# Kernel optimization log

Hardware: AMD Instinct MI355X
Metric: run time of the kernel (lower is better)

Reference implementation:

```python
import jax, jax.numpy as jnp
import numpy as np

CHANNELS = 512
GROUPS = 32
EPS = 1e-6


def setup_inputs() -> dict:
    key = jax.random.key(0)
    ks = jax.random.split(key, 10)
    C = CHANNELS
    s = 1.0 / np.sqrt(C)
    return {
        "hidden_states": jax.random.normal(ks[0], (4, 64, 64, C), dtype=jnp.float32),
        "gn_scale": jnp.ones((C,), dtype=jnp.float32),
        "gn_bias": jnp.zeros((C,), dtype=jnp.float32),
        "wq": jax.random.normal(ks[1], (C, C), dtype=jnp.float32) * s,
        "bq": jnp.zeros((C,), dtype=jnp.float32),
        "wk": jax.random.normal(ks[2], (C, C), dtype=jnp.float32) * s,
        "bk": jnp.zeros((C,), dtype=jnp.float32),
        "wv": jax.random.normal(ks[3], (C, C), dtype=jnp.float32) * s,
        "bv": jnp.zeros((C,), dtype=jnp.float32),
        "wo": jax.random.normal(ks[4], (C, C), dtype=jnp.float32) * s,
        "bo": jnp.zeros((C,), dtype=jnp.float32),
    }


def reference(hidden_states, gn_scale, gn_bias, wq, bq, wk, bk, wv, bv, wo, bo):
    B, H, W, C = hidden_states.shape
    residual = hidden_states
    L = H * W
    x = hidden_states.reshape(B, L, C)

    # GroupNorm: stats over (spatial, channels-within-group), per batch per group
    xg = x.reshape(B, L, GROUPS, C // GROUPS)
    mean = jnp.mean(xg, axis=(1, 3), keepdims=True)
    var = jnp.var(xg, axis=(1, 3), keepdims=True)
    xn = ((xg - mean) * jax.lax.rsqrt(var + EPS)).reshape(B, L, C)
    xn = xn * gn_scale + gn_bias

    # QKV projections (heads=1, head_dim=C)
    q = xn @ wq + bq
    k = xn @ wk + bk
    v = xn @ wv + bv

    scale = 1.0 / jnp.sqrt(jnp.asarray(C, dtype=q.dtype))
    scores = jnp.einsum('bld,bsd->bls', q, k) * scale  # [B, L, L]
    attn = jax.nn.softmax(scores, axis=-1)
    out = jnp.einsum('bls,bsd->bld', attn, v)

    out = out @ wo + bo
    return out.reshape(B, H, W, C) + residual
```

## Files before the change

kernel.cpp:

```cpp
#include <hip/hip_runtime.h>
#include <hip/hip_bf16.h>
#include <stdint.h>

#define BATCH 4
#define SEQ   4096
#define CH    512
#define NGRP  32
#define GEPS  1e-6f

typedef short  short8  __attribute__((ext_vector_type(8)));
typedef float  floatx4 __attribute__((ext_vector_type(4)));
typedef long   longx2  __attribute__((ext_vector_type(2)));

static __device__ __forceinline__ short bf16b(float f) {
    __hip_bfloat16 h = __float2bfloat16(f);
    return __builtin_bit_cast(short, h);
}
static __device__ __forceinline__ float bf2f(short s) {
    unsigned u = ((unsigned)(unsigned short)s) << 16;
    return __builtin_bit_cast(float, u);
}
static __device__ __forceinline__ char fp8b(float f) {
    int pk = __builtin_amdgcn_cvt_pk_fp8_f32(f, f, 0, false);
    return (char)(pk & 0xff);
}

static __device__ __forceinline__ void dma16(const void* g, void* l) {
    __builtin_amdgcn_global_load_lds(
        (const __attribute__((address_space(1))) unsigned int*)g,
        (__attribute__((address_space(3))) unsigned int*)l, 16, 0, 0);
}

static __device__ __forceinline__ float rowmax16(float x) {
    int xi = __builtin_bit_cast(int, x);
    x = fmaxf(x, __builtin_bit_cast(float, __builtin_amdgcn_update_dpp(xi, xi, 0x128, 0xf, 0xf, true)));
    xi = __builtin_bit_cast(int, x);
    x = fmaxf(x, __builtin_bit_cast(float, __builtin_amdgcn_update_dpp(xi, xi, 0x124, 0xf, 0xf, true)));
    xi = __builtin_bit_cast(int, x);
    x = fmaxf(x, __builtin_bit_cast(float, __builtin_amdgcn_update_dpp(xi, xi, 0x122, 0xf, 0xf, true)));
    xi = __builtin_bit_cast(int, x);
    x = fmaxf(x, __builtin_bit_cast(float, __builtin_amdgcn_update_dpp(xi, xi, 0x121, 0xf, 0xf, true)));
    return x;
}

__global__ __launch_bounds__(256) void gn_partial_kernel(const float* __restrict__ x,
                                                         float* __restrict__ statsraw) {
    int blk = blockIdx.x;
    int t = threadIdx.x;
    size_t row0 = (size_t)blk * 64;
    int qd = t & 127;
    int rh = t >> 7;
    const float* base = x + row0 * 512 + qd * 4;
    float s1 = 0.f, s2 = 0.f;
    #pragma unroll 4
    for (int i = 0; i < 32; ++i) {
        int r = rh + i * 2;
        float4 v = *reinterpret_cast<const float4*>(base + (size_t)r * 512);
        s1 += v.x + v.y + v.z + v.w;
        s2 += v.x * v.x + v.y * v.y + v.z * v.z + v.w * v.w;
    }
    __shared__ float a1[256], a2[256];
    a1[t] = s1; a2[t] = s2;
    __syncthreads();
    if (t < 32) {
        float u1 = 0.f, u2 = 0.f;
        #pragma unroll
        for (int e = 0; e < 4; ++e) {
            u1 += a1[t * 4 + e] + a1[128 + t * 4 + e];
            u2 += a2[t * 4 + e] + a2[128 + t * 4 + e];
        }
        int b = (int)(row0 >> 12);
        atomicAdd(&statsraw[(b * 32 + t) * 2],     u1);
        atomicAdd(&statsraw[(b * 32 + t) * 2 + 1], u2);
    }
}

__global__ __launch_bounds__(256) void gn_apply_kernel(const float* __restrict__ x,
                                                       const float* __restrict__ statsraw,
                                                       const float* __restrict__ gsc,
                                                       const float* __restrict__ gbs,
                                                       short* __restrict__ xn) {
    int i4 = blockIdx.x * 256 + threadIdx.x;
    int base = i4 * 4;
    int b = base >> 21;
    int c = base & 511;
    int sidx = (b * 32 + (c >> 4)) * 2;
    float s1 = statsraw[sidx], s2 = statsraw[sidx + 1];
    float mean = s1 * (1.f / 65536.f);
    float var  = s2 * (1.f / 65536.f) - mean * mean;
    float rstd = rsqrtf(var + GEPS);
    float4 xv = reinterpret_cast<const float4*>(x)[i4];
    float4 sv = *reinterpret_cast<const float4*>(gsc + c);
    float4 bv = *reinterpret_cast<const float4*>(gbs + c);
    union { short s[4]; uint2 u; } p;
    p.s[0] = bf16b((xv.x - mean) * rstd * sv.x + bv.x);
    p.s[1] = bf16b((xv.y - mean) * rstd * sv.y + bv.y);
    p.s[2] = bf16b((xv.z - mean) * rstd * sv.z + bv.z);
    p.s[3] = bf16b((xv.w - mean) * rstd * sv.w + bv.w);
    reinterpret_cast<uint2*>(xn)[i4] = p.u;
}

__global__ __launch_bounds__(256) void wtrans_kernel(const float* __restrict__ w0,
                                                     const float* __restrict__ w1,
                                                     const float* __restrict__ w2,
                                                     const float* __restrict__ w3,
                                                     short* __restrict__ wT) {
    const float* w = (blockIdx.z == 0) ? w0 : (blockIdx.z == 1) ? w1
                   : (blockIdx.z == 2) ? w2 : w3;
    short* out = wT + (size_t)blockIdx.z * CH * CH;
    int n0 = blockIdx.x * 32, k0 = blockIdx.y * 32;
    int tx = threadIdx.x, ty = threadIdx.y;
    __shared__ float s[32][33];
    #pragma unroll
    for (int i = 0; i < 4; ++i) {
        int kk = ty + i * 8;
        s[kk][tx] = w[(size_t)(k0 + kk) * CH + n0 + tx];
    }
    __syncthreads();
    #pragma unroll
    for (int i = 0; i < 4; ++i) {
        int nn = ty + i * 8;
        out[(size_t)(n0 + nn) * CH + k0 + tx] = bf16b(s[tx][nn]);
    }
}

__global__ __launch_bounds__(256) void gemm_qkv_kernel(const short* __restrict__ A,
                                                       const short* __restrict__ wT,
                                                       const float* __restrict__ bq,
                                                       const float* __restrict__ bk,
                                                       const float* __restrict__ bv,
                                                       char* __restrict__ q8,
                                                       char* __restrict__ k8,
                                                       char* __restrict__ vT8) {
    __shared__ short As[128 * 64];
    __shared__ short Bs[128 * 64];
    __shared__ char  vls[128 * 144];
    int m0 = blockIdx.x * 128;
    int nblk = blockIdx.y;
    int which = nblk >> 2;
    int n0 = (nblk & 3) * 128;
    const short* BT = wT + (size_t)which * 512 * 512;
    const float* bias = (which == 0) ? bq : (which == 1) ? bk : bv;
    int t = threadIdx.x;
    int w = t >> 6, lane = t & 63;
    int wr = w >> 1, wc = w & 1;
    int l15 = lane & 15, l4 = lane >> 4;
    floatx4 acc[4][4];
    #pragma unroll
    for (int i = 0; i < 4; ++i)
        #pragma unroll
        for (int j = 0; j < 4; ++j) acc[i][j] = (floatx4){0.f, 0.f, 0.f, 0.f};

    for (int k0 = 0; k0 < 512; k0 += 64) {
        __syncthreads();
        #pragma unroll
        for (int i = 0; i < 4; ++i) {
            int c = i * 256 + t;
            int row = c >> 3, j = (c & 7) ^ (row & 7);
            dma16(&A[(size_t)(m0 + row) * 512 + k0 + j * 8], &As[(c & ~63) * 8]);
            dma16(&BT[(size_t)(n0 + row) * 512 + k0 + j * 8], &Bs[(c & ~63) * 8]);
        }
        __syncthreads();
        #pragma unroll
        for (int kk = 0; kk < 64; kk += 32) {
            short8 af[4], bf[4];
            #pragma unroll
            for (int i = 0; i < 4; ++i) {
                int row = wr * 64 + i * 16 + l15;
                int j = (kk >> 3) + l4;
                af[i] = *reinterpret_cast<const short8*>(&As[(row * 8 + (j ^ (l15 & 7))) * 8]);
            }
            #pragma unroll
            for (int j2 = 0; j2 < 4; ++j2) {
                int row = wc * 64 + j2 * 16 + l15;
                int j = (kk >> 3) + l4;
                bf[j2] = *reinterpret_cast<const short8*>(&Bs[(row * 8 + (j ^ (l15 & 7))) * 8]);
            }
            #pragma unroll
            for (int i = 0; i < 4; ++i)
                #pragma unroll
                for (int j2 = 0; j2 < 4; ++j2)
                    acc[i][j2] = __builtin_amdgcn_mfma_f32_16x16x32_bf16(af[i], bf[j2], acc[i][j2], 0, 0, 0);
        }
    }
    if (which == 0) {
        #pragma unroll
        for (int i = 0; i < 4; ++i)
            #pragma unroll
            for (int j = 0; j < 4; ++j)
                #pragma unroll
                for (int r = 0; r < 4; ++r) {
                    int row = m0 + wr * 64 + i * 16 + l4 * 4 + r;
                    int col = n0 + wc * 64 + j * 16 + l15;
                    q8[(size_t)row * 512 + col] = fp8b(acc[i][j][r] + bias[col]);
                }
    } else if (which == 1) {
        #pragma unroll
        for (int i = 0; i < 4; ++i)
            #pragma unroll
            for (int j = 0; j < 4; ++j)
                #pragma unroll
                for (int r = 0; r < 4; ++r) {
                    int row = m0 + wr * 64 + i * 16 + l4 * 4 + r;
                    int col = n0 + wc * 64 + j * 16 + l15;
                    int bb = row >> 12, s = row & 4095;
                    size_t idx = (size_t)bb * 2097152 + (size_t)(s >> 5) * 16384
                               + (s & 15) * 1024 + ((s >> 4) & 1) * 8
                               + (col >> 3) * 16 + (col & 7);
                    k8[idx] = fp8b(acc[i][j][r] + bias[col]);
                }
    } else {
        __syncthreads();
        #pragma unroll
        for (int i = 0; i < 4; ++i)
            #pragma unroll
            for (int j = 0; j < 4; ++j)
                #pragma unroll
                for (int r = 0; r < 4; ++r) {
                    int rl = wr * 64 + i * 16 + l4 * 4 + r;
                    int rp = (rl & ~31) | (((rl & 15) << 1) | ((rl >> 4) & 1));
                    int cl = wc * 64 + j * 16 + l15;
                    vls[cl * 144 + rp] = fp8b(acc[i][j][r] + bias[n0 + cl]);
                }
        __syncthreads();
        int b = m0 >> 12, l0 = m0 & 4095;
        #pragma unroll
        for (int p = 0; p < 4; ++p) {
            int slot = p * 256 + t;
            int c = slot >> 3, off = (slot & 7) * 16;
            uint4 v;
            __builtin_memcpy(&v, &vls[c * 144 + off], 16);
            int dcol = n0 + c;
            int g = dcol >> 5, rr = dcol & 15, h = (dcol >> 4) & 1;
            int s = l0 + off;
            int sb = s >> 5, mb = (s & 31) >> 3;
            char* dst = vT8 + (size_t)b * 2097152 + (size_t)sb * 16384
                      + (size_t)((((g * 16 + rr) * 4 + mb) * 16) + h * 8);
            unsigned long long lo = ((unsigned long long)v.y << 32) | v.x;
            unsigned long long hi = ((unsigned long long)v.w << 32) | v.z;
            *reinterpret_cast<unsigned long long*>(dst)      = lo;
            *reinterpret_cast<unsigned long long*>(dst + 16) = hi;
        }
    }
}

__global__ __launch_bounds__(256) void gemm_bt_kernel(const short* __restrict__ Opart,
                                                      const float* __restrict__ ml,
                                                      const short* __restrict__ BT,
                                                      const float* __restrict__ bias,
                                                      float* __restrict__ outf,
                                                      const float* __restrict__ resid) {
    __shared__ short As[128 * 64];
    __shared__ short Bs[128 * 64];
    int m0 = blockIdx.x * 128, n0 = blockIdx.y * 128;
    int t = threadIdx.x;
    int w = t >> 6, lane = t & 63;
    int wr = w >> 1, wc = w & 1;
    int l15 = lane & 15, l4 = lane >> 4;
    const size_t PART = (size_t)BATCH * SEQ;
    floatx4 acc[4][4];
    #pragma unroll
    for (int i = 0; i < 4; ++i)
        #pragma unroll
        for (int j = 0; j < 4; ++j) acc[i][j] = (floatx4){0.f, 0.f, 0.f, 0.f};

    for (int k0 = 0; k0 < 512; k0 += 64) {
        __syncthreads();
        #pragma unroll
        for (int i = 0; i < 4; ++i) {
            int c = i * 256 + t;
            int rl = c >> 3, j = (c & 7) ^ (rl & 7);
            size_t rowg = (size_t)(m0 + rl);
            const short* s0 = Opart + rowg * 512 + k0 + j * 8;
            const short* s1 = s0 + PART * 512;
            uint4 a0 = *reinterpret_cast<const uint4*>(s0);
            uint4 a1 = *reinterpret_cast<const uint4*>(s1);
            float mA = ml[rowg * 2],          lA = ml[rowg * 2 + 1];
            float mB = ml[(PART + rowg) * 2], lB = ml[(PART + rowg) * 2 + 1];
            float mm = fmaxf(mA, mB);
            float e0 = __expf(mA - mm), e1 = __expf(mB - mm);
            float inv = 1.f / (e0 * lA + e1 * lB);
            e0 *= inv; e1 *= inv;
            union { uint4 u; short s[8]; } ua, ub, uo;
            ua.u = a0; ub.u = a1;
            #pragma unroll
            for (int e = 0; e < 8; ++e)
                uo.s[e] = bf16b(bf2f(ua.s[e]) * e0 + bf2f(ub.s[e]) * e1);
            *reinterpret_cast<uint4*>(&As[c * 8]) = uo.u;
            dma16(&BT[(size_t)(n0 + rl) * 512 + k0 + j * 8], &Bs[(c & ~63) * 8]);
        }
        __syncthreads();
        #pragma unroll
        for (int kk = 0; kk < 64; kk += 32) {
            short8 af[4], bf[4];
            #pragma unroll
            for (int i = 0; i < 4; ++i) {
                int row = wr * 64 + i * 16 + l15;
                int j = (kk >> 3) + l4;
                af[i] = *reinterpret_cast<const short8*>(&As[(row * 8 + (j ^ (l15 & 7))) * 8]);
            }
            #pragma unroll
            for (int j2 = 0; j2 < 4; ++j2) {
                int row = wc * 64 + j2 * 16 + l15;
                int j = (kk >> 3) + l4;
                bf[j2] = *reinterpret_cast<const short8*>(&Bs[(row * 8 + (j ^ (l15 & 7))) * 8]);
            }
            #pragma unroll
            for (int i = 0; i < 4; ++i)
                #pragma unroll
                for (int j2 = 0; j2 < 4; ++j2)
                    acc[i][j2] = __builtin_amdgcn_mfma_f32_16x16x32_bf16(af[i], bf[j2], acc[i][j2], 0, 0, 0);
        }
    }
    #pragma unroll
    for (int i = 0; i < 4; ++i)
        #pragma unroll
        for (int j = 0; j < 4; ++j)
            #pragma unroll
            for (int r = 0; r < 4; ++r) {
                int row = m0 + wr * 64 + i * 16 + l4 * 4 + r;
                int col = n0 + wc * 64 + j * 16 + l15;
                float vv = acc[i][j][r] + bias[col];
                outf[(size_t)row * 512 + col] = vv + resid[(size_t)row * 512 + col];
            }
}

__global__ __launch_bounds__(256, 2) void flash_kernel(const char* __restrict__ q8,
                                                       const char* __restrict__ k8,
                                                       const char* __restrict__ v8,
                                                       short* __restrict__ Opart,
                                                       float* __restrict__ ml) {
    __shared__ __align__(16) char smem[68096];
    int bx = blockIdx.x;
    int pb = bx & 7;
    int part = pb >> 2, b = pb & 3;
    int q0 = (bx >> 3) * 64;
    int t = threadIdx.x, w = t >> 6, lane = t & 63;
    int l15 = lane & 15, l4 = lane >> 4;
    const float scale = 0.044194173824159216f;

    long qf[16];
    {
        const char* qrow = q8 + ((size_t)b * SEQ + q0 + w * 16 + l15) * 512;
        #pragma unroll
        for (int ks = 0; ks < 16; ++ks)
            qf[ks] = *reinterpret_cast<const long*>(qrow + ks * 32 + l4 * 8);
    }

    floatx4 acc[32];
    #pragma unroll
    for (int i = 0; i < 32; ++i) acc[i] = (floatx4){0.f, 0.f, 0.f, 0.f};
    floatx4 lacc = (floatx4){0.f, 0.f, 0.f, 0.f};
    float mused[4] = {-1e30f, -1e30f, -1e30f, -1e30f};

    const long ones = 0x3838383838383838L;

    const char* kbase = k8 + (size_t)b * SEQ * 512;
    const char* vbase = v8 + (size_t)b * 512 * SEQ;

    const int ksw = l15 & 7;
    const int vsw = (l15 >> 1) & 3;
    const int sb0 = part * 64;

    auto stage = [&](int sb, int buf) {
        char* Kd = smem + buf * 16384;
        char* Vd = smem + 32768 + buf * 16384;
        const char* kt = kbase + (size_t)sb * 16384;
        const char* vt = vbase + (size_t)sb * 16384;
        #pragma unroll
        for (int i = 0; i < 4; ++i) {
            int c = i * 256 + t;
            int src = (c & ~63) | ((c & 63) ^ ((c >> 6) & 7));
            dma16(kt + (size_t)src * 16, Kd + (size_t)(c & ~63) * 16);
        }
        #pragma unroll
        for (int i = 0; i < 4; ++i) {
            int c = i * 256 + t;
            int src = (c & ~3) | ((c & 3) ^ ((c >> 3) & 3));
            dma16(vt + (size_t)src * 16, Vd + (size_t)(c & ~63) * 16);
        }
    };

    stage(sb0, 0);
    __syncthreads();

    for (int it = 0; it < 64; ++it) {
        int cur = it & 1;
        if (it + 1 < 64) stage(sb0 + it + 1, 1 - cur);

        const char* Kb = smem + cur * 16384;
        const char* Vb = smem + 32768 + cur * 16384;

        floatx4 sa0 = (floatx4){0.f, 0.f, 0.f, 0.f};
        floatx4 sa1 = (floatx4){0.f, 0.f, 0.f, 0.f};
        #pragma unroll
        for (int ks = 0; ks < 16; ++ks) {
            longx2 kk = *reinterpret_cast<const longx2*>(
                Kb + ((l15 * 64 + ((ks * 4 + l4) ^ ksw)) << 4));
            sa0 = __builtin_amdgcn_mfma_f32_16x16x32_fp8_fp8(qf[ks], kk[0], sa0, 0, 0, 0);
            sa1 = __builtin_amdgcn_mfma_f32_16x16x32_fp8_fp8(qf[ks], kk[1], sa1, 0, 0, 0);
        }

        float v0[4], v1[4], nm4[4];
        bool need = false;
        #pragma unroll
        for (int r = 0; r < 4; ++r) {
            v0[r] = sa0[r] * scale; v1[r] = sa1[r] * scale;
            nm4[r] = rowmax16(fmaxf(v0[r], v1[r]));
            need |= (nm4[r] > mused[r] + 5.0f);
        }
        if (__ballot(need)) {
            #pragma unroll
            for (int r = 0; r < 4; ++r) {
                float nm = fmaxf(mused[r], nm4[r]);
                float al = __expf(mused[r] - nm);
                lacc[r] *= al;
                #pragma unroll
                for (int i = 0; i < 32; ++i) acc[i][r] *= al;
                mused[r] = nm;
            }
        }
        float p0[4], p1[4];
        #pragma unroll
        for (int r = 0; r < 4; ++r) {
            p0[r] = __expf(v0[r] - mused[r]);
            p1[r] = __expf(v1[r] - mused[r]);
        }

        char* Ps = smem + 65536 + w * 640;
        #pragma unroll
        for (int r = 0; r < 4; ++r) {
            int pk = __builtin_amdgcn_cvt_pk_fp8_f32(p0[r], p1[r], 0, false);
            *reinterpret_cast<short*>(Ps + (l4 * 4 + r) * 40 + l15 * 2) = (short)pk;
        }

        long pf;
        __builtin_memcpy(&pf, (const char*)__builtin_assume_aligned(Ps + l15 * 40 + l4 * 8, 8), 8);
        lacc = __builtin_amdgcn_mfma_f32_16x16x32_fp8_fp8(pf, ones, lacc, 0, 0, 0);
        #pragma unroll
        for (int g = 0; g < 16; ++g) {
            longx2 vv = *reinterpret_cast<const longx2*>(
                Vb + ((((g * 16 + l15) * 4) + (l4 ^ vsw)) << 4));
            acc[2 * g]     = __builtin_amdgcn_mfma_f32_16x16x32_fp8_fp8(pf, vv[0], acc[2 * g],     0, 0, 0);
            acc[2 * g + 1] = __builtin_amdgcn_mfma_f32_16x16x32_fp8_fp8(pf, vv[1], acc[2 * g + 1], 0, 0, 0);
        }

        __syncthreads();
    }

    short* obase = Opart + (((size_t)part * BATCH + b) * SEQ + q0 + w * 16) * 512;
    #pragma unroll
    for (int r = 0; r < 4; ++r) {
        #pragma unroll
        for (int tt = 0; tt < 32; ++tt)
            obase[(size_t)(l4 * 4 + r) * 512 + tt * 16 + l15] = bf16b(acc[tt][r]);
    }
    if (l15 == 0) {
        #pragma unroll
        for (int r = 0; r < 4; ++r) {
            size_t rowg = ((size_t)part * BATCH + b) * SEQ + q0 + w * 16 + l4 * 4 + r;
            ml[rowg * 2]     = mused[r];
            ml[rowg * 2 + 1] = lacc[r];
        }
    }
}

extern "C" void kernel_launch(void* const* d_in, const int* in_sizes, int n_in,
                              void* d_out, int out_size, void* d_ws, size_t ws_size,
                              hipStream_t stream) {
    const float* x   = (const float*)d_in[0];
    const float* gsc = (const float*)d_in[1];
    const float* gbs = (const float*)d_in[2];
    const float* wq  = (const float*)d_in[3];
    const float* bq  = (const float*)d_in[4];
    const float* wk  = (const float*)d_in[5];
    const float* bk  = (const float*)d_in[6];
    const float* wv  = (const float*)d_in[7];
    const float* bv  = (const float*)d_in[8];
    const float* wo  = (const float*)d_in[9];
    const float* bo  = (const float*)d_in[10];
    float* out = (float*)d_out;

    char* ws = (char*)d_ws;
    const size_t MB = 1ull << 20;
    short* xn    = (short*)ws;
    char*  q8    = (char*)(ws + 16 * MB);
    char*  k8    = (char*)(ws + 24 * MB);
    char*  vT8   = (char*)(ws + 32 * MB);
    short* Opart = (short*)(ws + 40 * MB);
    short* wT    = (short*)(ws + 72 * MB);
    float* stats = (float*)(ws + 74 * MB);
    float* ml    = (float*)(ws + 74 * MB + 65536);

    hipMemsetAsync(stats, 0, 256 * sizeof(float), stream);
    gn_partial_kernel<<<256, 256, 0, stream>>>(x, stats);
    gn_apply_kernel<<<8192, 256, 0, stream>>>(x, stats, gsc, gbs, xn);
    wtrans_kernel<<<dim3(16, 16, 4), dim3(32, 8), 0, stream>>>(wq, wk, wv, wo, wT);

    short* woT = wT + 786432;

    gemm_qkv_kernel<<<dim3(128, 12), 256, 0, stream>>>(xn, wT, bq, bk, bv, q8, k8, vT8);
    flash_kernel<<<512, 256, 0, stream>>>(q8, k8, vT8, Opart, ml);
    gemm_bt_kernel<<<dim3(128, 4), 256, 0, stream>>>(Opart, ml, woT, bo, out, x);
}
```

Measured before the change: 289.0 us.

## Software-pipeline flash attention: overlap QK^T of next tile with PV of current

```diff
diff --git a/kernel.cpp b/kernel.cpp
--- a/kernel.cpp
+++ b/kernel.cpp
@@ -278,7 +278,7 @@
             float mA = ml[rowg * 2],          lA = ml[rowg * 2 + 1];
             float mB = ml[(PART + rowg) * 2], lB = ml[(PART + rowg) * 2 + 1];
             float mm = fmaxf(mA, mB);
-            float e0 = __expf(mA - mm), e1 = __expf(mB - mm);
+            float e0 = exp2f(mA - mm), e1 = exp2f(mB - mm);
             float inv = 1.f / (e0 * lA + e1 * lB);
             e0 *= inv; e1 *= inv;
             union { uint4 u; short s[8]; } ua, ub, uo;
@@ -337,7 +337,8 @@
     int q0 = (bx >> 3) * 64;
     int t = threadIdx.x, w = t >> 6, lane = t & 63;
     int l15 = lane & 15, l4 = lane >> 4;
-    const float scale = 0.044194173824159216f;
+    const float c2 = 0.06375873735f;
+    const float MARGIN = 7.2134752f;
 
     long qf[16];
     {
@@ -357,22 +358,27 @@
 
     const char* kbase = k8 + (size_t)b * SEQ * 512;
     const char* vbase = v8 + (size_t)b * 512 * SEQ;
+    const int sb0 = part * 64;
 
     const int ksw = l15 & 7;
     const int vsw = (l15 >> 1) & 3;
-    const int sb0 = part * 64;
-
-    auto stage = [&](int sb, int buf) {
-        char* Kd = smem + buf * 16384;
-        char* Vd = smem + 32768 + buf * 16384;
+    const char* kAddrE = smem + ((l15 * 64 + (l4 ^ ksw)) << 4);
+    const char* kAddrO = smem + ((l15 * 64 + ((4 + l4) ^ ksw)) << 4);
+    const int vLane = (l15 * 4 + (l4 ^ vsw)) << 4;
+    char* Ps = smem + 65536 + w * 640;
+
+    auto stageK = [&](int sb) {
         const char* kt = kbase + (size_t)sb * 16384;
-        const char* vt = vbase + (size_t)sb * 16384;
         #pragma unroll
         for (int i = 0; i < 4; ++i) {
             int c = i * 256 + t;
             int src = (c & ~63) | ((c & 63) ^ ((c >> 6) & 7));
-            dma16(kt + (size_t)src * 16, Kd + (size_t)(c & ~63) * 16);
-        }
+            dma16(kt + (size_t)src * 16, smem + (size_t)(c & ~63) * 16);
+        }
+    };
+    auto stageV = [&](int sb, int vOff) {
+        const char* vt = vbase + (size_t)sb * 16384;
+        char* Vd = smem + vOff;
         #pragma unroll
         for (int i = 0; i < 4; ++i) {
             int c = i * 256 + t;
@@ -380,73 +386,99 @@
             dma16(vt + (size_t)src * 16, Vd + (size_t)(c & ~63) * 16);
         }
     };
-
-    stage(sb0, 0);
-    __syncthreads();
-
-    for (int it = 0; it < 64; ++it) {
-        int cur = it & 1;
-        if (it + 1 < 64) stage(sb0 + it + 1, 1 - cur);
-
-        const char* Kb = smem + cur * 16384;
-        const char* Vb = smem + 32768 + cur * 16384;
-
-        floatx4 sa0 = (floatx4){0.f, 0.f, 0.f, 0.f};
-        floatx4 sa1 = (floatx4){0.f, 0.f, 0.f, 0.f};
-        #pragma unroll
-        for (int ks = 0; ks < 16; ++ks) {
-            longx2 kk = *reinterpret_cast<const longx2*>(
-                Kb + ((l15 * 64 + ((ks * 4 + l4) ^ ksw)) << 4));
-            sa0 = __builtin_amdgcn_mfma_f32_16x16x32_fp8_fp8(qf[ks], kk[0], sa0, 0, 0, 0);
-            sa1 = __builtin_amdgcn_mfma_f32_16x16x32_fp8_fp8(qf[ks], kk[1], sa1, 0, 0, 0);
-        }
-
+    auto qkt = [&](floatx4& sa0, floatx4& sa1) {
+        __builtin_amdgcn_s_setprio(1);
+        #pragma unroll
+        for (int j = 0; j < 8; ++j) {
+            longx2 kE = *reinterpret_cast<const longx2*>(kAddrE + j * 128);
+            longx2 kO = *reinterpret_cast<const longx2*>(kAddrO + j * 128);
+            sa0 = __builtin_amdgcn_mfma_f32_16x16x32_fp8_fp8(qf[2 * j],     kE[0], sa0, 0, 0, 0);
+            sa1 = __builtin_amdgcn_mfma_f32_16x16x32_fp8_fp8(qf[2 * j],     kE[1], sa1, 0, 0, 0);
+            sa0 = __builtin_amdgcn_mfma_f32_16x16x32_fp8_fp8(qf[2 * j + 1], kO[0], sa0, 0, 0, 0);
+            sa1 = __builtin_amdgcn_mfma_f32_16x16x32_fp8_fp8(qf[2 * j + 1], kO[1], sa1, 0, 0, 0);
+        }
+        __builtin_amdgcn_s_setprio(0);
+    };
+    auto pv = [&](long pfv, int vRd) {
+        __builtin_amdgcn_s_setprio(1);
+        lacc = __builtin_amdgcn_mfma_f32_16x16x32_fp8_fp8(pfv, ones, lacc, 0, 0, 0);
+        const char* Vb = smem + vRd;
+        #pragma unroll
+        for (int g = 0; g < 16; ++g) {
+            longx2 vv = *reinterpret_cast<const longx2*>(Vb + vLane + g * 1024);
+            acc[2 * g]     = __builtin_amdgcn_mfma_f32_16x16x32_fp8_fp8(pfv, vv[0], acc[2 * g],     0, 0, 0);
+            acc[2 * g + 1] = __builtin_amdgcn_mfma_f32_16x16x32_fp8_fp8(pfv, vv[1], acc[2 * g + 1], 0, 0, 0);
+        }
+        __builtin_amdgcn_s_setprio(0);
+    };
+    auto softmax = [&](floatx4 sa0, floatx4 sa1) -> long {
         float v0[4], v1[4], nm4[4];
         bool need = false;
         #pragma unroll
         for (int r = 0; r < 4; ++r) {
-            v0[r] = sa0[r] * scale; v1[r] = sa1[r] * scale;
+            v0[r] = sa0[r] * c2; v1[r] = sa1[r] * c2;
             nm4[r] = rowmax16(fmaxf(v0[r], v1[r]));
-            need |= (nm4[r] > mused[r] + 5.0f);
+            need |= (nm4[r] > mused[r] + MARGIN);
+        }
+        #pragma unroll
+        for (int r = 0; r < 4; ++r) {
+            int pk = __builtin_amdgcn_cvt_pk_fp8_f32(exp2f(v0[r] - mused[r]),
+                                                     exp2f(v1[r] - mused[r]), 0, false);
+            *reinterpret_cast<short*>(Ps + (l4 * 4 + r) * 40 + l15 * 2) = (short)pk;
         }
         if (__ballot(need)) {
             #pragma unroll
             for (int r = 0; r < 4; ++r) {
                 float nm = fmaxf(mused[r], nm4[r]);
-                float al = __expf(mused[r] - nm);
+                float al = exp2f(mused[r] - nm);
                 lacc[r] *= al;
                 #pragma unroll
                 for (int i = 0; i < 32; ++i) acc[i][r] *= al;
                 mused[r] = nm;
+                int pk = __builtin_amdgcn_cvt_pk_fp8_f32(exp2f(v0[r] - nm),
+                                                         exp2f(v1[r] - nm), 0, false);
+                *reinterpret_cast<short*>(Ps + (l4 * 4 + r) * 40 + l15 * 2) = (short)pk;
             }
         }
-        float p0[4], p1[4];
-        #pragma unroll
-        for (int r = 0; r < 4; ++r) {
-            p0[r] = __expf(v0[r] - mused[r]);
-            p1[r] = __expf(v1[r] - mused[r]);
-        }
-
-        char* Ps = smem + 65536 + w * 640;
-        #pragma unroll
-        for (int r = 0; r < 4; ++r) {
-            int pk = __builtin_amdgcn_cvt_pk_fp8_f32(p0[r], p1[r], 0, false);
-            *reinterpret_cast<short*>(Ps + (l4 * 4 + r) * 40 + l15 * 2) = (short)pk;
-        }
-
-        long pf;
-        __builtin_memcpy(&pf, (const char*)__builtin_assume_aligned(Ps + l15 * 40 + l4 * 8, 8), 8);
-        lacc = __builtin_amdgcn_mfma_f32_16x16x32_fp8_fp8(pf, ones, lacc, 0, 0, 0);
-        #pragma unroll
-        for (int g = 0; g < 16; ++g) {
-            longx2 vv = *reinterpret_cast<const longx2*>(
-                Vb + ((((g * 16 + l15) * 4) + (l4 ^ vsw)) << 4));
-            acc[2 * g]     = __builtin_amdgcn_mfma_f32_16x16x32_fp8_fp8(pf, vv[0], acc[2 * g],     0, 0, 0);
-            acc[2 * g + 1] = __builtin_amdgcn_mfma_f32_16x16x32_fp8_fp8(pf, vv[1], acc[2 * g + 1], 0, 0, 0);
-        }
-
-        __syncthreads();
-    }
+        long pfv;
+        __builtin_memcpy(&pfv, (const char*)__builtin_assume_aligned(Ps + l15 * 40 + l4 * 8, 8), 8);
+        return pfv;
+    };
+
+    stageV(sb0, 16384);
+    stageK(sb0);
+    asm volatile("s_waitcnt vmcnt(0)" ::: "memory");
+    __syncthreads();
+
+    long pf;
+    {
+        stageV(sb0 + 1, 32768);
+        floatx4 sa0 = (floatx4){0.f, 0.f, 0.f, 0.f};
+        floatx4 sa1 = (floatx4){0.f, 0.f, 0.f, 0.f};
+        qkt(sa0, sa1);
+        __syncthreads();
+        stageK(sb0 + 1);
+        pf = softmax(sa0, sa1);
+        asm volatile("s_waitcnt vmcnt(0)" ::: "memory");
+        __syncthreads();
+    }
+    int vRd = 16384;
+    int vWr = 49152;
+    for (int it = 1; it < 64; ++it) {
+        if (it + 1 < 64) stageV(sb0 + it + 1, vWr);
+        floatx4 sa0 = (floatx4){0.f, 0.f, 0.f, 0.f};
+        floatx4 sa1 = (floatx4){0.f, 0.f, 0.f, 0.f};
+        qkt(sa0, sa1);
+        __syncthreads();
+        if (it + 1 < 64) stageK(sb0 + it + 1);
+        pv(pf, vRd);
+        pf = softmax(sa0, sa1);
+        asm volatile("s_waitcnt vmcnt(0)" ::: "memory");
+        __syncthreads();
+        vRd = (vRd == 49152) ? 16384 : vRd + 16384;
+        vWr = (vWr == 49152) ? 16384 : vWr + 16384;
+    }
+    pv(pf, vRd);
 
     short* obase = Opart + (((size_t)part * BATCH + b) * SEQ + q0 + w * 16) * 512;
     #pragma unroll
```

After: 294.8 us. +2.0%, slower.

## Use exp2 softmax, precompute LDS addresses, and raise MFMA wave priority

Applied to the files above, without the earlier changes.

```diff
diff --git a/kernel.cpp b/kernel.cpp
--- a/kernel.cpp
+++ b/kernel.cpp
@@ -278,7 +278,7 @@
             float mA = ml[rowg * 2],          lA = ml[rowg * 2 + 1];
             float mB = ml[(PART + rowg) * 2], lB = ml[(PART + rowg) * 2 + 1];
             float mm = fmaxf(mA, mB);
-            float e0 = __expf(mA - mm), e1 = __expf(mB - mm);
+            float e0 = exp2f(mA - mm), e1 = exp2f(mB - mm);
             float inv = 1.f / (e0 * lA + e1 * lB);
             e0 *= inv; e1 *= inv;
             union { uint4 u; short s[8]; } ua, ub, uo;
@@ -337,7 +337,8 @@
     int q0 = (bx >> 3) * 64;
     int t = threadIdx.x, w = t >> 6, lane = t & 63;
     int l15 = lane & 15, l4 = lane >> 4;
-    const float scale = 0.044194173824159216f;
+    const float c2 = 0.06375873735f;
+    const float MARGIN = 7.2134752f;
 
     long qf[16];
     {
@@ -357,28 +358,33 @@
 
     const char* kbase = k8 + (size_t)b * SEQ * 512;
     const char* vbase = v8 + (size_t)b * 512 * SEQ;
+    const int sb0 = part * 64;
 
     const int ksw = l15 & 7;
     const int vsw = (l15 >> 1) & 3;
-    const int sb0 = part * 64;
+    const char* kA_E = smem + ((l15 * 64 + (l4 ^ ksw)) << 4);
+    const char* kA_O = smem + ((l15 * 64 + ((4 + l4) ^ ksw)) << 4);
+    const char* vA   = smem + 32768 + ((l15 * 4 + (l4 ^ vsw)) << 4);
+    char* Ps = smem + 65536 + w * 640;
+
+    int kSrc[4], vSrc[4];
+    #pragma unroll
+    for (int i = 0; i < 4; ++i) {
+        int c = i * 256 + t;
+        kSrc[i] = (((c & ~63) | ((c & 63) ^ ((c >> 6) & 7))) << 4);
+        vSrc[i] = (((c & ~3)  | ((c & 3)  ^ ((c >> 3) & 3))) << 4);
+    }
+    const int ldsD = (t & ~63) << 4;
 
     auto stage = [&](int sb, int buf) {
-        char* Kd = smem + buf * 16384;
-        char* Vd = smem + 32768 + buf * 16384;
         const char* kt = kbase + (size_t)sb * 16384;
         const char* vt = vbase + (size_t)sb * 16384;
-        #pragma unroll
-        for (int i = 0; i < 4; ++i) {
-            int c = i * 256 + t;
-            int src = (c & ~63) | ((c & 63) ^ ((c >> 6) & 7));
-            dma16(kt + (size_t)src * 16, Kd + (size_t)(c & ~63) * 16);
-        }
-        #pragma unroll
-        for (int i = 0; i < 4; ++i) {
-            int c = i * 256 + t;
-            int src = (c & ~3) | ((c & 3) ^ ((c >> 3) & 3));
-            dma16(vt + (size_t)src * 16, Vd + (size_t)(c & ~63) * 16);
-        }
+        char* Kd = smem + buf * 16384 + ldsD;
+        char* Vd = smem + 32768 + buf * 16384 + ldsD;
+        #pragma unroll
+        for (int i = 0; i < 4; ++i) dma16(kt + kSrc[i], Kd + i * 4096);
+        #pragma unroll
+        for (int i = 0; i < 4; ++i) dma16(vt + vSrc[i], Vd + i * 4096);
     };
 
     stage(sb0, 0);
@@ -386,64 +392,60 @@
 
     for (int it = 0; it < 64; ++it) {
         int cur = it & 1;
+        int coff = cur << 14;
         if (it + 1 < 64) stage(sb0 + it + 1, 1 - cur);
-
-        const char* Kb = smem + cur * 16384;
-        const char* Vb = smem + 32768 + cur * 16384;
 
         floatx4 sa0 = (floatx4){0.f, 0.f, 0.f, 0.f};
         floatx4 sa1 = (floatx4){0.f, 0.f, 0.f, 0.f};
-        #pragma unroll
-        for (int ks = 0; ks < 16; ++ks) {
-            longx2 kk = *reinterpret_cast<const longx2*>(
-                Kb + ((l15 * 64 + ((ks * 4 + l4) ^ ksw)) << 4));
-            sa0 = __builtin_amdgcn_mfma_f32_16x16x32_fp8_fp8(qf[ks], kk[0], sa0, 0, 0, 0);
-            sa1 = __builtin_amdgcn_mfma_f32_16x16x32_fp8_fp8(qf[ks], kk[1], sa1, 0, 0, 0);
-        }
+        __builtin_amdgcn_s_setprio(1);
+        #pragma unroll
+        for (int j = 0; j < 8; ++j) {
+            longx2 kE = *reinterpret_cast<const longx2*>(kA_E + coff + j * 128);
+            longx2 kO = *reinterpret_cast<const longx2*>(kA_O + coff + j * 128);
+            sa0 = __builtin_amdgcn_mfma_f32_16x16x32_fp8_fp8(qf[2 * j],     kE[0], sa0, 0, 0, 0);
+            sa1 = __builtin_amdgcn_mfma_f32_16x16x32_fp8_fp8(qf[2 * j],     kE[1], sa1, 0, 0, 0);
+            sa0 = __builtin_amdgcn_mfma_f32_16x16x32_fp8_fp8(qf[2 * j + 1], kO[0], sa0, 0, 0, 0);
+            sa1 = __builtin_amdgcn_mfma_f32_16x16x32_fp8_fp8(qf[2 * j + 1], kO[1], sa1, 0, 0, 0);
+        }
+        __builtin_amdgcn_s_setprio(0);
 
         float v0[4], v1[4], nm4[4];
         bool need = false;
         #pragma unroll
         for (int r = 0; r < 4; ++r) {
-            v0[r] = sa0[r] * scale; v1[r] = sa1[r] * scale;
+            v0[r] = sa0[r] * c2; v1[r] = sa1[r] * c2;
             nm4[r] = rowmax16(fmaxf(v0[r], v1[r]));
-            need |= (nm4[r] > mused[r] + 5.0f);
+            need |= (nm4[r] > mused[r] + MARGIN);
         }
         if (__ballot(need)) {
             #pragma unroll
             for (int r = 0; r < 4; ++r) {
                 float nm = fmaxf(mused[r], nm4[r]);
-                float al = __expf(mused[r] - nm);
+                float al = exp2f(mused[r] - nm);
                 lacc[r] *= al;
                 #pragma unroll
                 for (int i = 0; i < 32; ++i) acc[i][r] *= al;
                 mused[r] = nm;
             }
         }
-        float p0[4], p1[4];
         #pragma unroll
         for (int r = 0; r < 4; ++r) {
-            p0[r] = __expf(v0[r] - mused[r]);
-            p1[r] = __expf(v1[r] - mused[r]);
-        }
-
-        char* Ps = smem + 65536 + w * 640;
-        #pragma unroll
-        for (int r = 0; r < 4; ++r) {
-            int pk = __builtin_amdgcn_cvt_pk_fp8_f32(p0[r], p1[r], 0, false);
+            int pk = __builtin_amdgcn_cvt_pk_fp8_f32(exp2f(v0[r] - mused[r]),
+                                                     exp2f(v1[r] - mused[r]), 0, false);
             *reinterpret_cast<short*>(Ps + (l4 * 4 + r) * 40 + l15 * 2) = (short)pk;
         }
 
         long pf;
         __builtin_memcpy(&pf, (const char*)__builtin_assume_aligned(Ps + l15 * 40 + l4 * 8, 8), 8);
+        __builtin_amdgcn_s_setprio(1);
         lacc = __builtin_amdgcn_mfma_f32_16x16x32_fp8_fp8(pf, ones, lacc, 0, 0, 0);
         #pragma unroll
         for (int g = 0; g < 16; ++g) {
-            longx2 vv = *reinterpret_cast<const longx2*>(
-                Vb + ((((g * 16 + l15) * 4) + (l4 ^ vsw)) << 4));
+            longx2 vv = *reinterpret_cast<const longx2*>(vA + coff + g * 1024);
             acc[2 * g]     = __builtin_amdgcn_mfma_f32_16x16x32_fp8_fp8(pf, vv[0], acc[2 * g],     0, 0, 0);
             acc[2 * g + 1] = __builtin_amdgcn_mfma_f32_16x16x32_fp8_fp8(pf, vv[1], acc[2 * g + 1], 0, 0, 0);
         }
+        __builtin_amdgcn_s_setprio(0);
 
         __syncthreads();
     }
```

Result: no change. 292.9 us (+1.3%).
